# Kernel optimization log

Measured on AMD Instinct MI355X. Metric: run time of the kernel, lower is better.

## Reference

```python
import jax, jax.numpy as jnp
import numpy as np

DIM = 2048      # model dim
H = 32          # num_heads
N = 128         # state_dim
G = 1           # num_groups
K = 4           # conv_size
HID = 4096     # hidden_dim = multiple_of*ceil(2.0*DIM/256)
P = HID // H    # head_dim = 128
CHUNK = 256
EPS = 1e-6
DT_MIN, DT_MAX = 0.001, 0.1


def setup_inputs() -> dict:
    key = jax.random.key(0)
    ks = jax.random.split(key, 8)
    b, s = 2, 2048
    d_in = 2 * HID + 2 * G * N + H           # 8448
    conv_dim = HID + 2 * G * N               # 4352
    return {
        "x": jax.random.normal(ks[0], (b, s, DIM), jnp.float32),
        "W_in": jax.random.normal(ks[1], (d_in, DIM), jnp.float32) / np.sqrt(DIM),
        "conv_w": jax.random.normal(ks[2], (conv_dim, K), jnp.float32) / np.sqrt(K),
        "conv_b": jnp.zeros((conv_dim,), jnp.float32),
        "dt_bias": jnp.zeros((H,), jnp.float32),
        "A_log": jnp.log(jax.random.uniform(ks[3], (H,), jnp.float32, 1.0, 16.0)),
        "D": jnp.ones((H,), jnp.float32),
        "norm_w": jnp.ones((HID,), jnp.float32),
        "W_out": jax.random.normal(ks[4], (DIM, HID), jnp.float32) / np.sqrt(HID),
    }


def _causal_conv_silu(xBC, w, bias):
    # depthwise causal conv1d, kernel K, then SiLU. xBC: (b,s,c), w: (c,K)
    b, s, c = xBC.shape
    xp = jnp.pad(xBC, ((0, 0), (K - 1, 0), (0, 0)))
    y = sum(xp[:, k:k + s, :] * w[:, k] for k in range(K)) + bias
    return jax.nn.silu(y)


def _chunked_scan(x, dt, A, B, C, D):
    # Mamba2 chunked selective scan.
    # x:(b,s,h,p) dt:(b,s,h) A:(h,) B,C:(b,s,n) (groups=1) D:(h,)
    b, s, h, p = x.shape
    n = B.shape[-1]
    nc, L = s // CHUNK, CHUNK
    xc = x.reshape(b, nc, L, h, p)
    dtc = dt.reshape(b, nc, L, h)
    Bc = B.reshape(b, nc, L, n)
    Cc = C.reshape(b, nc, L, n)

    dA = dtc * A                          # (b,nc,L,h), A<0
    dA_cs = jnp.cumsum(dA, axis=2)        # (b,nc,L,h)

    # intra-chunk contribution
    seg = dA_cs[:, :, :, None, :] - dA_cs[:, :, None, :, :]   # (b,nc,L,L,h)
    mask = jnp.tril(jnp.ones((L, L), bool))[None, None, :, :, None]
    decay = jnp.exp(jnp.where(mask, seg, -jnp.inf))
    CB = jnp.einsum('bcln,bcsn->bcls', Cc, Bc)                # (b,nc,L,L)
    y_intra = jnp.einsum('bcls,bclsh,bcsh,bcshp->bclhp', CB, decay, dtc, xc)

    # per-chunk final states
    decay_states = jnp.exp(dA_cs[:, :, -1:, :] - dA_cs)       # (b,nc,L,h)
    states = jnp.einsum('bclh,bclh,bclhp,bcln->bchpn', decay_states, dtc, xc, Bc)

    # inter-chunk recurrence over chunk index
    dA_chunk = dA_cs[:, :, -1, :]                              # (b,nc,h)
    def step(prev, inp):
        st, dec = inp
        new = prev * jnp.exp(dec)[:, :, None, None] + st
        return new, prev
    init = jnp.zeros((b, h, p, n), x.dtype)
    _, prev_states = jax.lax.scan(step, init,
                                  (jnp.moveaxis(states, 1, 0), jnp.moveaxis(dA_chunk, 1, 0)))
    prev_states = jnp.moveaxis(prev_states, 0, 1)              # state at start of each chunk

    y_inter = jnp.einsum('bcln,bclh,bchpn->bclhp', Cc, jnp.exp(dA_cs), prev_states)
    y = (y_intra + y_inter).reshape(b, s, h, p)
    return y + x * D[None, None, :, None]


def reference(x, W_in, conv_w, conv_b, dt_bias, A_log, D, norm_w, W_out):
    b, s, _ = x.shape
    zxbcdt = x @ W_in.T                                        # (b,s,2*HID+2GN+H)
    z, xBC, dt = jnp.split(zxbcdt, [HID, 2 * HID + 2 * G * N], axis=-1)
    xBC = _causal_conv_silu(xBC, conv_w, conv_b)
    xs, B, C = jnp.split(xBC, [HID, HID + G * N], axis=-1)
    A = -jnp.exp(A_log)
    dt = jnp.clip(jax.nn.softplus(dt + dt_bias), DT_MIN, DT_MAX)
    xs = xs.reshape(b, s, H, P)
    y = _chunked_scan(xs, dt, A, B, C, D).reshape(b, s, HID)
    y = y * jax.nn.silu(z)                                     # gate, norm_before_gate=False
    y = y * jax.lax.rsqrt(jnp.mean(y * y, axis=-1, keepdims=True) + EPS) * norm_w
    return y @ W_out.T
```

## Files before the change

kernel.cpp:

```cpp
#include <hip/hip_runtime.h>


typedef short s16x8 __attribute__((ext_vector_type(8)));
typedef float f32x4 __attribute__((ext_vector_type(4)));

__device__ __forceinline__ float bf2f(ushort u) {
    return __builtin_bit_cast(float, (unsigned)u << 16);
}
__device__ __forceinline__ ushort f2bf(float f) {
    unsigned u = __builtin_bit_cast(unsigned, f);
    unsigned r = u + 0x7fffu + ((u >> 16) & 1u);
    return (ushort)(r >> 16);
}

__device__ __forceinline__ void gld16(const void* g, void* l) {
    __builtin_amdgcn_global_load_lds((__attribute__((address_space(1))) void*)g,
                                     (__attribute__((address_space(3))) void*)l, 16, 0, 0);
}

#define BARRIER() asm volatile("s_barrier" ::: "memory")

__global__ void cast_all_k(const float4* __restrict__ x, const float4* __restrict__ wout,
                           const float4* __restrict__ win, ushort* __restrict__ xb,
                           ushort* __restrict__ woutb, ushort* __restrict__ winb) {
    const long b = blockIdx.x, tid = threadIdx.x;
    if (b < 8192) {
        long i = b * 256 + tid;
        float4 v = x[i];
        ushort4 o = { f2bf(v.x), f2bf(v.y), f2bf(v.z), f2bf(v.w) };
        *(ushort4*)(xb + i * 4) = o;
    } else if (b < 16384) {
        long i = (b - 8192) * 256 + tid;
        float4 v = wout[i];
        ushort4 o = { f2bf(v.x), f2bf(v.y), f2bf(v.z), f2bf(v.w) };
        *(ushort4*)(woutb + i * 4) = o;
    } else {
        long i = (b - 16384) * 256 + tid;
        ushort4 o;
        if (i < 4341760L) {
            float4 v = win[i];
            o = { f2bf(v.x), f2bf(v.y), f2bf(v.z), f2bf(v.w) };
        } else {
            o = { 0, 0, 0, 0 };
        }
        *(ushort4*)(winb + i * 4) = o;
    }
}

__global__ __launch_bounds__(512, 1) void gemm1_k(const ushort* __restrict__ A,
                                                  const ushort* __restrict__ Bm,
                                                  ushort* __restrict__ zbuf,
                                                  ushort* __restrict__ xbc,
                                                  ushort* __restrict__ dtr) {
    constexpr int K = 2048, NT = 64;
    __shared__ ushort lds[3 * 8192 + 3 * 6144];
    const int tid = threadIdx.x, lane = tid & 63, wave = tid >> 6;
    const int wm = wave >> 2, wn = wave & 3;
    const int bid = blockIdx.x;
    const int xcd = bid & 7, w = bid >> 3;
    const int mt = xcd * 2 + (w & 1), nt = w >> 1;
    const long m0 = (long)mt * 256, n0 = (long)nt * 192;

    const int st_row = lane >> 2;
    const int st_gc = ((lane & 3) * 8) ^ (((lane >> 5) & 1) << 4);

    auto STAGE_A = [&](int buf, int kt) {
#pragma unroll
        for (int j = 0; j < 2; j++) {
            int sidx = wave + j * 8;
            gld16(A + (m0 + sidx * 16 + st_row) * K + kt + st_gc,
                  lds + buf * 8192 + sidx * 512 + lane * 8);
        }
    };
    auto STAGE_B = [&](int buf, int kt) {
#pragma unroll
        for (int j = 0; j < 2; j++) {
            int sidx = wave + j * 8;
            if (sidx < 12)
                gld16(Bm + (n0 + sidx * 16 + st_row) * K + kt + st_gc,
                      lds + 24576 + buf * 6144 + sidx * 512 + lane * 8);
        }
    };

    const int cfr = (lane >> 4) * 8;
    const int lr = lane & 15;
    auto LDFA = [&](int buf, int r) -> s16x8 {
        int off = buf * 8192 + ((r >> 4) << 9) + ((r & 15) << 5)
                + (cfr ^ (((r >> 3) & 1) << 4));
        return *(const s16x8*)(lds + off);
    };
    auto LDFB = [&](int buf, int r) -> s16x8 {
        int off = 24576 + buf * 6144 + ((r >> 4) << 9) + ((r & 15) << 5)
                + (cfr ^ (((r >> 3) & 1) << 4));
        return *(const s16x8*)(lds + off);
    };

    f32x4 zero = { 0.f, 0.f, 0.f, 0.f };
    f32x4 acc[8][3];
#pragma unroll
    for (int i = 0; i < 8; i++)
#pragma unroll
        for (int j = 0; j < 3; j++) acc[i][j] = zero;

    STAGE_A(0, 0);  STAGE_B(0, 0);
    STAGE_A(1, 32); STAGE_B(1, 32);
    asm volatile("s_waitcnt vmcnt(3)" ::: "memory");
    BARRIER();

    for (int t = 0; t < NT; ++t) {
        const int cur = t % 3;
        const int nxt = (t + 2) % 3;
        const int kt2 = (t + 2) * 32;
        const bool do_stage = (t + 2) < NT;

        s16x8 bfr[3], alo[4], ahi[4];
#pragma unroll
        for (int ni = 0; ni < 3; ni++) bfr[ni] = LDFB(cur, wn * 48 + ni * 16 + lr);
#pragma unroll
        for (int mi = 0; mi < 4; mi++) alo[mi] = LDFA(cur, wm * 128 + mi * 16 + lr);
#pragma unroll
        for (int mi = 0; mi < 4; mi++) ahi[mi] = LDFA(cur, wm * 128 + 64 + mi * 16 + lr);
        if (do_stage) { STAGE_A(nxt, kt2); STAGE_B(nxt, kt2); }

        __builtin_amdgcn_s_setprio(1);
#pragma unroll
        for (int mi = 0; mi < 4; mi++)
#pragma unroll
            for (int ni = 0; ni < 3; ni++)
                acc[mi][ni] = __builtin_amdgcn_mfma_f32_16x16x32_bf16(alo[mi], bfr[ni], acc[mi][ni], 0, 0, 0);
#pragma unroll
        for (int mi = 0; mi < 4; mi++)
#pragma unroll
            for (int ni = 0; ni < 3; ni++)
                acc[mi + 4][ni] = __builtin_amdgcn_mfma_f32_16x16x32_bf16(ahi[mi], bfr[ni], acc[mi + 4][ni], 0, 0, 0);
        __builtin_amdgcn_s_setprio(0);

        if (do_stage) asm volatile("s_waitcnt vmcnt(3)" ::: "memory");
        else          asm volatile("s_waitcnt vmcnt(0)" ::: "memory");
        BARRIER();
    }

    const int lr4 = (lane >> 4) * 4;
#pragma unroll
    for (int mi = 0; mi < 8; mi++) {
#pragma unroll
        for (int ni = 0; ni < 3; ni++) {
            const long col = n0 + wn * 48 + ni * 16 + lr;
            ushort* dst;
            long stride;
            if (col < 4096)      { dst = zbuf + col;         stride = 4096; }
            else if (col < 8448) { dst = xbc + (col - 4096); stride = 4352; }
            else if (col < 8480) { dst = dtr + (col - 8448); stride = 32;   }
            else continue;
            const long row0 = m0 + wm * 128 + mi * 16 + lr4;
#pragma unroll
            for (int r = 0; r < 4; r++) dst[(row0 + r) * stride] = f2bf(acc[mi][ni][r]);
        }
    }
}

__global__ __launch_bounds__(512, 1) void gemm2_k(const ushort* __restrict__ A,
                                                  const ushort* __restrict__ Bm,
                                                  float* __restrict__ Cout) {
    constexpr int K = 4096, NT = 128;
    __shared__ ushort lds[3 * 8192 + 3 * 4096];
    const int tid = threadIdx.x, lane = tid & 63, wave = tid >> 6;
    const int wm = wave >> 2, wn = wave & 3;
    const int bid = blockIdx.x;
    const int xcd = bid & 7, w = bid >> 3;
    const int mt = xcd * 2 + (w & 1), nt = w >> 1;
    const long m0 = (long)mt * 256, n0 = (long)nt * 128;

    const int st_row = lane >> 2;
    const int st_gc = ((lane & 3) * 8) ^ (((lane >> 5) & 1) << 4);

    auto STAGE_A = [&](int buf, int kt) {
#pragma unroll
        for (int j = 0; j < 2; j++) {
            int sidx = wave + j * 8;
            gld16(A + (m0 + sidx * 16 + st_row) * K + kt + st_gc,
                  lds + buf * 8192 + sidx * 512 + lane * 8);
        }
    };
    auto STAGE_B = [&](int buf, int kt) {
        int sidx = wave;
        gld16(Bm + (n0 + sidx * 16 + st_row) * K + kt + st_gc,
              lds + 24576 + buf * 4096 + sidx * 512 + lane * 8);
    };

    const int cfr = (lane >> 4) * 8;
    const int lr = lane & 15;
    auto LDFA = [&](int buf, int r) -> s16x8 {
        int off = buf * 8192 + ((r >> 4) << 9) + ((r & 15) << 5)
                + (cfr ^ (((r >> 3) & 1) << 4));
        return *(const s16x8*)(lds + off);
    };
    auto LDFB = [&](int buf, int r) -> s16x8 {
        int off = 24576 + buf * 4096 + ((r >> 4) << 9) + ((r & 15) << 5)
                + (cfr ^ (((r >> 3) & 1) << 4));
        return *(const s16x8*)(lds + off);
    };

    f32x4 zero = { 0.f, 0.f, 0.f, 0.f };
    f32x4 acc[8][2];
#pragma unroll
    for (int i = 0; i < 8; i++)
#pragma unroll
        for (int j = 0; j < 2; j++) acc[i][j] = zero;

    STAGE_A(0, 0);  STAGE_B(0, 0);
    STAGE_A(1, 32); STAGE_B(1, 32);
    asm volatile("s_waitcnt vmcnt(2)" ::: "memory");
    BARRIER();

    for (int t = 0; t < NT; ++t) {
        const int cur = t % 3;
        const int nxt = (t + 2) % 3;
        const int kt2 = (t + 2) * 32;
        const bool do_stage = (t + 2) < NT;

        s16x8 bfr[2], alo[4], ahi[4];
#pragma unroll
        for (int ni = 0; ni < 2; ni++) bfr[ni] = LDFB(cur, wn * 32 + ni * 16 + lr);
#pragma unroll
        for (int mi = 0; mi < 4; mi++) alo[mi] = LDFA(cur, wm * 128 + mi * 16 + lr);
#pragma unroll
        for (int mi = 0; mi < 4; mi++) ahi[mi] = LDFA(cur, wm * 128 + 64 + mi * 16 + lr);
        if (do_stage) { STAGE_A(nxt, kt2); STAGE_B(nxt, kt2); }

        __builtin_amdgcn_s_setprio(1);
#pragma unroll
        for (int mi = 0; mi < 4; mi++)
#pragma unroll
            for (int ni = 0; ni < 2; ni++)
                acc[mi][ni] = __builtin_amdgcn_mfma_f32_16x16x32_bf16(alo[mi], bfr[ni], acc[mi][ni], 0, 0, 0);
#pragma unroll
        for (int mi = 0; mi < 4; mi++)
#pragma unroll
            for (int ni = 0; ni < 2; ni++)
                acc[mi + 4][ni] = __builtin_amdgcn_mfma_f32_16x16x32_bf16(ahi[mi], bfr[ni], acc[mi + 4][ni], 0, 0, 0);
        __builtin_amdgcn_s_setprio(0);

        if (do_stage) asm volatile("s_waitcnt vmcnt(2)" ::: "memory");
        else          asm volatile("s_waitcnt vmcnt(0)" ::: "memory");
        BARRIER();
    }

    const int lr4 = (lane >> 4) * 4;
#pragma unroll
    for (int mi = 0; mi < 8; mi++) {
#pragma unroll
        for (int ni = 0; ni < 2; ni++) {
            const long col = n0 + wn * 32 + ni * 16 + lr;
            const long row0 = m0 + wm * 128 + mi * 16 + lr4;
#pragma unroll
            for (int r = 0; r < 4; r++)
                Cout[(row0 + r) * 2048 + col] = acc[mi][ni][r];
        }
    }
}

__global__ __launch_bounds__(256) void convx_k(const ushort* __restrict__ xbc,
                                               const float* __restrict__ w,
                                               const float* __restrict__ bias,
                                               ushort* __restrict__ xbcc,
                                               ushort* __restrict__ xT,
                                               ushort* __restrict__ Bt) {
    __shared__ ushort xin[35][136];
    __shared__ ushort yL[32][132];
    const int stile = blockIdx.x, slot = blockIdx.y, bc = blockIdx.z;
    const int tid = threadIdx.x;
    const int cc = bc & 7;
    const long tbase = (long)bc * 256 + stile * 32;
    const int c0 = slot * 128;
    const bool head = (cc == 0 && stile == 0);

#pragma unroll
    for (int i = 0; i < 3; i++) {
        int u = tid + i * 256;
        if (u < 560) {
            int r = u >> 4, seg = u & 15;
            s16x8 v;
            if (head && r < 3) {
#pragma unroll
                for (int j = 0; j < 8; j++) v[j] = 0;
            } else {
                v = *(const s16x8*)&xbc[(tbase - 3 + r) * 4352 + c0 + seg * 8];
            }
            *(s16x8*)&xin[r][seg * 8] = v;
        }
    }
    __syncthreads();

    const int s_loc = tid >> 3, p0 = (tid & 7) * 16;
    ushort yo[16];
#pragma unroll
    for (int j = 0; j < 16; j++) {
        int c = p0 + j;
        float a = bias[c0 + c];
#pragma unroll
        for (int k = 0; k < 4; k++)
            a += bf2f(xin[s_loc + k][c]) * w[(c0 + c) * 4 + k];
        float yv = a / (1.f + __expf(-a));
        ushort ub = f2bf(yv);
        yo[j] = ub;
        yL[s_loc][c] = ub;
    }
    *(s16x8*)&xbcc[(tbase + s_loc) * 4352 + c0 + p0] = *(const s16x8*)&yo[0];
    *(s16x8*)&xbcc[(tbase + s_loc) * 4352 + c0 + p0 + 8] = *(const s16x8*)&yo[8];
    __syncthreads();

    if (slot < 33) {
        const int p = tid >> 1, s0 = (tid & 1) * 16;
        ushort o[16];
#pragma unroll
        for (int j = 0; j < 16; j++) o[j] = yL[s0 + j][p];
        ushort* dst = (slot < 32)
            ? (xT + ((long)(bc * 32 + slot) * 128 + p) * 256 + stile * 32 + s0)
            : (Bt + ((long)bc * 128 + p) * 256 + stile * 32 + s0);
        *(s16x8*)&dst[0] = *(const s16x8*)&o[0];
        *(s16x8*)&dst[8] = *(const s16x8*)&o[8];
    }
}

__global__ void prep_k(const ushort* __restrict__ dtr, const float* __restrict__ dt_bias,
                       const float* __restrict__ A_log, float* __restrict__ dtp,
                       float* __restrict__ dacs) {
    const int bx = blockIdx.x;
    const int h = bx & 31, cc = (bx >> 5) & 7, bi = bx >> 8;
    const int lane = threadIdx.x;
    const float A = -__expf(A_log[h]);
    const float bsh = dt_bias[h];
    float v[4], cs[4];
    float run = 0.f;
#pragma unroll
    for (int j = 0; j < 4; j++) {
        int pos = cc * 256 + lane * 4 + j;
        float raw = bf2f(dtr[((long)(bi * 2048 + pos)) * 32 + h]) + bsh;
        float sp = (raw > 20.f) ? raw : log1pf(__expf(raw));
        float d = fminf(fmaxf(sp, 0.001f), 0.1f);
        v[j] = d;
        run += d * A;
        cs[j] = run;
    }
    float tot = run, pre = run;
    for (int off = 1; off < 64; off <<= 1) {
        float u = __shfl_up(pre, off, 64);
        if (lane >= off) pre += u;
    }
    float excl = pre - tot;
    const long base = ((long)(bi * 32 + h)) * 2048 + cc * 256 + lane * 4;
#pragma unroll
    for (int j = 0; j < 4; j++) { dtp[base + j] = v[j]; dacs[base + j] = excl + cs[j]; }
}

__global__ __launch_bounds__(256) void cb_mfma_k(const ushort* __restrict__ xbcc,
                                                 float* __restrict__ CB) {
    const int bid = blockIdx.x;
    const int sq = bid & 1, lq = (bid >> 1) & 1, bc = bid >> 2;
    const int tid = threadIdx.x, lane = tid & 63, wave = tid >> 6;
    const int wm = wave >> 1, wn = wave & 1;
    const long tbase = (long)bc * 256;

    f32x4 zero = { 0.f, 0.f, 0.f, 0.f };
    f32x4 acc[4][4];
#pragma unroll
    for (int i = 0; i < 4; i++)
#pragma unroll
        for (int j = 0; j < 4; j++) acc[i][j] = zero;

    for (int kst = 0; kst < 4; ++kst) {
        const int koff = kst * 32 + (lane >> 4) * 8;
        s16x8 a[4], b[4];
#pragma unroll
        for (int mi = 0; mi < 4; mi++) {
            int l = lq * 128 + wm * 64 + mi * 16 + (lane & 15);
            a[mi] = *(const s16x8*)&xbcc[(tbase + l) * 4352 + 4224 + koff];
        }
#pragma unroll
        for (int ni = 0; ni < 4; ni++) {
            int s = sq * 128 + wn * 64 + ni * 16 + (lane & 15);
            b[ni] = *(const s16x8*)&xbcc[(tbase + s) * 4352 + 4096 + koff];
        }
#pragma unroll
        for (int mi = 0; mi < 4; mi++)
#pragma unroll
            for (int ni = 0; ni < 4; ni++)
                acc[mi][ni] = __builtin_amdgcn_mfma_f32_16x16x32_bf16(a[mi], b[ni], acc[mi][ni], 0, 0, 0);
    }

    float* out = CB + (long)bc * 65536;
#pragma unroll
    for (int mi = 0; mi < 4; mi++)
#pragma unroll
        for (int ni = 0; ni < 4; ni++)
#pragma unroll
            for (int r = 0; r < 4; r++) {
                int l = lq * 128 + wm * 64 + mi * 16 + (lane >> 4) * 4 + r;
                int s = sq * 128 + wn * 64 + ni * 16 + (lane & 15);
                out[(long)l * 256 + s] = acc[mi][ni][r];
            }
}

__global__ __launch_bounds__(256) void scan_mfma_k(const ushort* __restrict__ xT,
                                                   const float* __restrict__ CB,
                                                   const float* __restrict__ dtp,
                                                   const float* __restrict__ dacs,
                                                   const ushort* __restrict__ xbcc,
                                                   const float* __restrict__ st,
                                                   float* __restrict__ yf) {
    const int bx = blockIdx.x;
    const int ltile = bx & 1, h = (bx >> 1) & 31, cc = (bx >> 6) & 7, bi = bx >> 9;
    const int tid = threadIdx.x, lane = tid & 63, wave = tid >> 6;
    const int wm = wave >> 1, wn = wave & 1;

    __shared__ float dA_s[256];
    __shared__ float F_s[256];

    const long dbase = ((long)(bi * 32 + h)) * 2048 + cc * 256;
    {
        float a = dacs[dbase + tid];
        float r = dacs[dbase + (tid | 31)];
        dA_s[tid] = a;
        F_s[tid] = __expf(r - a) * dtp[dbase + tid];
    }
    __syncthreads();

    int lch[4];
    float dAl[4];
#pragma unroll
    for (int mi = 0; mi < 4; mi++) {
        lch[mi] = ltile * 128 + wm * 64 + mi * 16 + (lane & 15);
        dAl[mi] = dA_s[lch[mi]];
    }

    f32x4 zero = { 0.f, 0.f, 0.f, 0.f };
    f32x4 acc[4][4];
#pragma unroll
    for (int i = 0; i < 4; i++)
#pragma unroll
        for (int j = 0; j < 4; j++) acc[i][j] = zero;

    const long tbase = (long)bi * 2048 + cc * 256;
    const long cbbase = ((long)(bi * 8 + cc)) * 65536;
    const ushort* xrow = xT + (((long)(bi * 8 + cc) * 32 + h) * 128) * 256;
    const int nsb = ltile * 4 + 4;

    for (int sb = 0; sb < nsb; ++sb) {
        const int soff = sb * 32 + (lane >> 4) * 8;
        s16x8 bf[4];
#pragma unroll
        for (int ni = 0; ni < 4; ni++) {
            int p = wn * 64 + ni * 16 + (lane & 15);
            bf[ni] = *(const s16x8*)&xrow[(long)p * 256 + soff];
        }
        const float Rsb = dA_s[sb * 32 + 31];
        const int s0 = soff;
#pragma unroll
        for (int mi = 0; mi < 4; mi++) {
            const int lb = lch[mi] >> 5;
            if (sb > lb) continue;
            const float* cbrow = CB + cbbase + (long)lch[mi] * 256 + s0;
            float4 c0 = *(const float4*)cbrow;
            float4 c1 = *(const float4*)(cbrow + 4);
            float E = __expf(dAl[mi] - Rsb);
            float m[8];
            m[0] = c0.x * E * F_s[s0 + 0]; m[1] = c0.y * E * F_s[s0 + 1];
            m[2] = c0.z * E * F_s[s0 + 2]; m[3] = c0.w * E * F_s[s0 + 3];
            m[4] = c1.x * E * F_s[s0 + 4]; m[5] = c1.y * E * F_s[s0 + 5];
            m[6] = c1.z * E * F_s[s0 + 6]; m[7] = c1.w * E * F_s[s0 + 7];
            if (sb == lb) {
#pragma unroll
                for (int j = 0; j < 8; j++)
                    if (s0 + j > lch[mi]) m[j] = 0.f;
            }
            s16x8 a;
#pragma unroll
            for (int j = 0; j < 8; j++) a[j] = (short)f2bf(m[j]);
#pragma unroll
            for (int ni = 0; ni < 4; ni++)
                acc[mi][ni] = __builtin_amdgcn_mfma_f32_16x16x32_bf16(a, bf[ni], acc[mi][ni], 0, 0, 0);
        }
    }

    const float* sbase = st + (((long)(bi * 8 + cc) * 32 + h) * 128) * 128;
    float eAr[4];
#pragma unroll
    for (int mi = 0; mi < 4; mi++) eAr[mi] = __expf(dAl[mi]);
    for (int kk = 0; kk < 4; ++kk) {
        const int koff = kk * 32 + (lane >> 4) * 8;
        s16x8 a[4], b[4];
#pragma unroll
        for (int mi = 0; mi < 4; mi++) {
            s16x8 raw = *(const s16x8*)&xbcc[(tbase + lch[mi]) * 4352 + 4224 + koff];
#pragma unroll
            for (int j = 0; j < 8; j++)
                a[mi][j] = (short)f2bf(bf2f((ushort)raw[j]) * eAr[mi]);
        }
#pragma unroll
        for (int ni = 0; ni < 4; ni++) {
            int p = wn * 64 + ni * 16 + (lane & 15);
            const float* pr = sbase + (long)p * 128 + koff;
            float4 v0 = *(const float4*)pr;
            float4 v1 = *(const float4*)(pr + 4);
            b[ni][0] = (short)f2bf(v0.x); b[ni][1] = (short)f2bf(v0.y);
            b[ni][2] = (short)f2bf(v0.z); b[ni][3] = (short)f2bf(v0.w);
            b[ni][4] = (short)f2bf(v1.x); b[ni][5] = (short)f2bf(v1.y);
            b[ni][6] = (short)f2bf(v1.z); b[ni][7] = (short)f2bf(v1.w);
        }
#pragma unroll
        for (int mi = 0; mi < 4; mi++)
#pragma unroll
            for (int ni = 0; ni < 4; ni++)
                acc[mi][ni] = __builtin_amdgcn_mfma_f32_16x16x32_bf16(a[mi], b[ni], acc[mi][ni], 0, 0, 0);
    }

    const long crow = tbase + ltile * 128 + wm * 64 + ((lane >> 4) << 2);
    const int ccol = h * 128 + wn * 64 + (lane & 15);
#pragma unroll
    for (int mi = 0; mi < 4; mi++)
#pragma unroll
        for (int ni = 0; ni < 4; ni++)
#pragma unroll
            for (int r = 0; r < 4; r++)
                yf[(crow + mi * 16 + r) * 4096 + ccol + ni * 16] = acc[mi][ni][r];
}

__global__ __launch_bounds__(256) void states_mfma_k(const ushort* __restrict__ xT,
                                                     const ushort* __restrict__ Bt,
                                                     const float* __restrict__ dtp,
                                                     const float* __restrict__ dacs,
                                                     float* __restrict__ states) {
    const int bx = blockIdx.x;
    const int h = bx & 31, cc = (bx >> 5) & 7, bi = bx >> 8;
    const int bc = bi * 8 + cc;
    const int tid = threadIdx.x, lane = tid & 63, wave = tid >> 6;
    const int wm = wave >> 1, wn = wave & 1;
    __shared__ float wl[256];
    const long dbase = ((long)(bi * 32 + h)) * 2048 + cc * 256;
    {
        float last = dacs[dbase + 255];
        wl[tid] = __expf(last - dacs[dbase + tid]) * dtp[dbase + tid];
    }
    __syncthreads();

    f32x4 zero = { 0.f, 0.f, 0.f, 0.f };
    f32x4 acc[4][4];
#pragma unroll
    for (int i = 0; i < 4; i++)
#pragma unroll
        for (int j = 0; j < 4; j++) acc[i][j] = zero;

    const ushort* xrow = xT + (((long)bc * 32 + h) * 128) * 256;
    const ushort* brow = Bt + ((long)bc * 128) * 256;

    for (int sb = 0; sb < 8; ++sb) {
        const int soff = sb * 32 + (lane >> 4) * 8;
        s16x8 a[4], b[4];
#pragma unroll
        for (int mi = 0; mi < 4; mi++) {
            int p = wm * 64 + mi * 16 + (lane & 15);
            s16x8 raw = *(const s16x8*)&xrow[(long)p * 256 + soff];
#pragma unroll
            for (int j = 0; j < 8; j++)
                a[mi][j] = (short)f2bf(bf2f((ushort)raw[j]) * wl[soff + j]);
        }
#pragma unroll
        for (int ni = 0; ni < 4; ni++) {
            int n = wn * 64 + ni * 16 + (lane & 15);
            b[ni] = *(const s16x8*)&brow[(long)n * 256 + soff];
        }
#pragma unroll
        for (int mi = 0; mi < 4; mi++)
#pragma unroll
            for (int ni = 0; ni < 4; ni++)
                acc[mi][ni] = __builtin_amdgcn_mfma_f32_16x16x32_bf16(a[mi], b[ni], acc[mi][ni], 0, 0, 0);
    }

    float* out = states + (((long)bc * 32 + h) * 128) * 128;
#pragma unroll
    for (int mi = 0; mi < 4; mi++)
#pragma unroll
        for (int ni = 0; ni < 4; ni++)
#pragma unroll
            for (int r = 0; r < 4; r++) {
                int p = wm * 64 + mi * 16 + (lane >> 4) * 4 + r;
                int n = wn * 64 + ni * 16 + (lane & 15);
                out[(long)p * 128 + n] = acc[mi][ni][r];
            }
}

__global__ void rec_k(float* __restrict__ states, const float* __restrict__ dacs) {
    const int i = blockIdx.x * 256 + threadIdx.x;
    const int n = i & 127, p = (i >> 7) & 127, h = (i >> 14) & 31, bi = i >> 19;
    const long dbase = ((long)(bi * 32 + h)) * 2048;
    float run = 0.f;
    for (int cc = 0; cc < 8; cc++) {
        const long off = ((((long)(bi * 8 + cc)) * 32 + h) * 128 + p) * 128 + n;
        float st = states[off];
        states[off] = run;
        float dec = dacs[dbase + cc * 256 + 255];
        run = run * __expf(dec) + st;
    }
}

__global__ __launch_bounds__(256) void gate_rms_k(const float* __restrict__ y, const ushort* __restrict__ zbuf,
                                                  const ushort* __restrict__ xbcc, const float* __restrict__ Dv,
                                                  const float* __restrict__ norm_w, ushort* __restrict__ yb) {
    const int t = blockIdx.x, tid = threadIdx.x;
    const float* yr = &y[(long)t * 4096];
    const ushort* zr = &zbuf[(long)t * 4096];
    const ushort* xr = &xbcc[(long)t * 4352];
    float g[16];
    float ss = 0.f;
#pragma unroll
    for (int j = 0; j < 16; j++) {
        int i = j * 256 + tid;
        float z = bf2f(zr[i]);
        float yv = yr[i] + Dv[i >> 7] * bf2f(xr[i]);
        float gv = yv * (z / (1.f + __expf(-z)));
        g[j] = gv;
        ss += gv * gv;
    }
#pragma unroll
    for (int off = 32; off > 0; off >>= 1) ss += __shfl_xor(ss, off, 64);
    __shared__ float red[4];
    if ((tid & 63) == 0) red[tid >> 6] = ss;
    __syncthreads();
    float tot = red[0] + red[1] + red[2] + red[3];
    float sc = rsqrtf(tot * (1.f / 4096.f) + 1e-6f);
#pragma unroll
    for (int j = 0; j < 16; j++) {
        int i = j * 256 + tid;
        yb[(long)t * 4096 + i] = f2bf(g[j] * sc * norm_w[i]);
    }
}

extern "C" void kernel_launch(void* const* d_in, const int* in_sizes, int n_in,
                              void* d_out, int out_size, void* d_ws, size_t ws_size,
                              hipStream_t stream) {
    const float* x       = (const float*)d_in[0];
    const float* W_in    = (const float*)d_in[1];
    const float* conv_w  = (const float*)d_in[2];
    const float* conv_b  = (const float*)d_in[3];
    const float* dt_bias = (const float*)d_in[4];
    const float* A_log   = (const float*)d_in[5];
    const float* Dv      = (const float*)d_in[6];
    const float* norm_w  = (const float*)d_in[7];
    const float* W_out   = (const float*)d_in[8];

    char* w8 = (char*)d_ws;
    ushort* xb    = (ushort*)(w8 + 0L);
    ushort* xT    = (ushort*)(w8 + 0L);
    ushort* yb    = (ushort*)(w8 + 0L);
    ushort* woutb = (ushort*)(w8 + 33554432L);
    ushort* Bt    = (ushort*)(w8 + 50331648L);
    ushort* zbuf  = (ushort*)(w8 + 52428800L);
    ushort* xbc   = (ushort*)(w8 + 85983232L);
    ushort* dtr   = (ushort*)(w8 + 121634816L);
    ushort* xbcc  = (ushort*)(w8 + 121896960L);
    float*  dtp   = (float*)(w8 + 157548544L);
    float*  dacs  = (float*)(w8 + 158072832L);
    float*  cb    = (float*)(w8 + 158597120L);
    float*  yf    = (float*)(w8 + 162791424L);
    ushort* winb  = (ushort*)(w8 + 162791424L);
    float*  st    = (float*)(w8 + 229900288L);

    cast_all_k<<<34048, 256, 0, stream>>>((const float4*)x, (const float4*)W_out,
                                          (const float4*)W_in, xb, woutb, winb);
    gemm1_k<<<736, 512, 0, stream>>>(xb, winb, zbuf, xbc, dtr);
    convx_k<<<dim3(8, 34, 16), 256, 0, stream>>>(xbc, conv_w, conv_b, xbcc, xT, Bt);
    prep_k<<<512, 64, 0, stream>>>(dtr, dt_bias, A_log, dtp, dacs);
    cb_mfma_k<<<64, 256, 0, stream>>>(xbcc, cb);
    states_mfma_k<<<512, 256, 0, stream>>>(xT, Bt, dtp, dacs, st);
    rec_k<<<4096, 256, 0, stream>>>(st, dacs);
    scan_mfma_k<<<1024, 256, 0, stream>>>(xT, cb, dtp, dacs, xbcc, st, yf);
    gate_rms_k<<<4096, 256, 0, stream>>>(yf, zbuf, xbcc, Dv, norm_w, yb);
    gemm2_k<<<256, 512, 0, stream>>>(yb, woutb, (float*)d_out);
}
```

Before: 465.1 us.

## Deepen GEMM LDS pipeline to four stages and double-buffer register fragments

Both projection GEMMs move from a 3-stage to a 4-stage LDS ring buffer, prefetching three K-tiles ahead. They also read the next tile's fragments from LDS into a second register set while MFMAs run on the current set. This is meant to hide global-load and LDS-read latency behind matrix math. The cost is more LDS and more VGPRs for the second fragment set, which may raise register pressure. Wait counts are now tuned per wave because of the uneven B-tile load split.

```diff
diff --git a/kernel.cpp b/kernel.cpp
--- a/kernel.cpp
+++ b/kernel.cpp
@@ -53,7 +53,7 @@
                                                   ushort* __restrict__ xbc,
                                                   ushort* __restrict__ dtr) {
     constexpr int K = 2048, NT = 64;
-    __shared__ ushort lds[3 * 8192 + 3 * 6144];
+    __shared__ ushort lds[4 * 8192 + 4 * 6144];
     const int tid = threadIdx.x, lane = tid & 63, wave = tid >> 6;
     const int wm = wave >> 2, wn = wave & 3;
     const int bid = blockIdx.x;
@@ -64,21 +64,19 @@
     const int st_row = lane >> 2;
     const int st_gc = ((lane & 3) * 8) ^ (((lane >> 5) & 1) << 4);
 
-    auto STAGE_A = [&](int buf, int kt) {
+    auto STAGE = [&](int buf, int kt) {
 #pragma unroll
         for (int j = 0; j < 2; j++) {
             int sidx = wave + j * 8;
             gld16(A + (m0 + sidx * 16 + st_row) * K + kt + st_gc,
                   lds + buf * 8192 + sidx * 512 + lane * 8);
         }
-    };
-    auto STAGE_B = [&](int buf, int kt) {
 #pragma unroll
         for (int j = 0; j < 2; j++) {
             int sidx = wave + j * 8;
             if (sidx < 12)
                 gld16(Bm + (n0 + sidx * 16 + st_row) * K + kt + st_gc,
-                      lds + 24576 + buf * 6144 + sidx * 512 + lane * 8);
+                      lds + 32768 + buf * 6144 + sidx * 512 + lane * 8);
         }
     };
 
@@ -90,10 +88,18 @@
         return *(const s16x8*)(lds + off);
     };
     auto LDFB = [&](int buf, int r) -> s16x8 {
-        int off = 24576 + buf * 6144 + ((r >> 4) << 9) + ((r & 15) << 5)
+        int off = 32768 + buf * 6144 + ((r >> 4) << 9) + ((r & 15) << 5)
                 + (cfr ^ (((r >> 3) & 1) << 4));
         return *(const s16x8*)(lds + off);
     };
+    auto RDFRAGS = [&](int buf, s16x8 (&f)[11]) {
+#pragma unroll
+        for (int ni = 0; ni < 3; ni++) f[ni] = LDFB(buf, wn * 48 + ni * 16 + lr);
+#pragma unroll
+        for (int mi = 0; mi < 4; mi++) f[3 + mi] = LDFA(buf, wm * 128 + mi * 16 + lr);
+#pragma unroll
+        for (int mi = 0; mi < 4; mi++) f[7 + mi] = LDFA(buf, wm * 128 + 64 + mi * 16 + lr);
+    };
 
     f32x4 zero = { 0.f, 0.f, 0.f, 0.f };
     f32x4 acc[8][3];
@@ -102,42 +108,45 @@
 #pragma unroll
         for (int j = 0; j < 3; j++) acc[i][j] = zero;
 
-    STAGE_A(0, 0);  STAGE_B(0, 0);
-    STAGE_A(1, 32); STAGE_B(1, 32);
-    asm volatile("s_waitcnt vmcnt(3)" ::: "memory");
+    auto MFMAS = [&](s16x8 (&f)[11]) {
+        __builtin_amdgcn_s_setprio(1);
+#pragma unroll
+        for (int mi = 0; mi < 4; mi++)
+#pragma unroll
+            for (int ni = 0; ni < 3; ni++)
+                acc[mi][ni] = __builtin_amdgcn_mfma_f32_16x16x32_bf16(f[3 + mi], f[ni], acc[mi][ni], 0, 0, 0);
+#pragma unroll
+        for (int mi = 0; mi < 4; mi++)
+#pragma unroll
+            for (int ni = 0; ni < 3; ni++)
+                acc[mi + 4][ni] = __builtin_amdgcn_mfma_f32_16x16x32_bf16(f[7 + mi], f[ni], acc[mi + 4][ni], 0, 0, 0);
+        __builtin_amdgcn_s_setprio(0);
+    };
+    auto VWAIT = [&](bool tail) {
+        if (tail)           { asm volatile("s_waitcnt vmcnt(0)" ::: "memory"); }
+        else if (wave < 4)  { asm volatile("s_waitcnt vmcnt(4)" ::: "memory"); }
+        else                { asm volatile("s_waitcnt vmcnt(3)" ::: "memory"); }
+    };
+
+    s16x8 fc[11], fn[11];
+
+    STAGE(0, 0); STAGE(1, 32); STAGE(2, 64);
+    VWAIT(false);
     BARRIER();
-
-    for (int t = 0; t < NT; ++t) {
-        const int cur = t % 3;
-        const int nxt = (t + 2) % 3;
-        const int kt2 = (t + 2) * 32;
-        const bool do_stage = (t + 2) < NT;
-
-        s16x8 bfr[3], alo[4], ahi[4];
-#pragma unroll
-        for (int ni = 0; ni < 3; ni++) bfr[ni] = LDFB(cur, wn * 48 + ni * 16 + lr);
-#pragma unroll
-        for (int mi = 0; mi < 4; mi++) alo[mi] = LDFA(cur, wm * 128 + mi * 16 + lr);
-#pragma unroll
-        for (int mi = 0; mi < 4; mi++) ahi[mi] = LDFA(cur, wm * 128 + 64 + mi * 16 + lr);
-        if (do_stage) { STAGE_A(nxt, kt2); STAGE_B(nxt, kt2); }
-
-        __builtin_amdgcn_s_setprio(1);
-#pragma unroll
-        for (int mi = 0; mi < 4; mi++)
-#pragma unroll
-            for (int ni = 0; ni < 3; ni++)
-                acc[mi][ni] = __builtin_amdgcn_mfma_f32_16x16x32_bf16(alo[mi], bfr[ni], acc[mi][ni], 0, 0, 0);
-#pragma unroll
-        for (int mi = 0; mi < 4; mi++)
-#pragma unroll
-            for (int ni = 0; ni < 3; ni++)
-                acc[mi + 4][ni] = __builtin_amdgcn_mfma_f32_16x16x32_bf16(ahi[mi], bfr[ni], acc[mi + 4][ni], 0, 0, 0);
-        __builtin_amdgcn_s_setprio(0);
-
-        if (do_stage) asm volatile("s_waitcnt vmcnt(3)" ::: "memory");
-        else          asm volatile("s_waitcnt vmcnt(0)" ::: "memory");
+    RDFRAGS(0, fc);
+
+    auto TILE = [&](int t, s16x8 (&cur)[11], s16x8 (&nxt)[11]) {
+        const bool do_stage = (t + 3) < NT;
+        if (do_stage) STAGE((t + 3) & 3, (t + 3) * 32);
+        if ((t + 1) < NT) RDFRAGS((t + 1) & 3, nxt);
+        MFMAS(cur);
+        VWAIT(!do_stage);
         BARRIER();
+    };
+
+    for (int t = 0; t < NT; t += 2) {
+        TILE(t, fc, fn);
+        TILE(t + 1, fn, fc);
     }
 
     const int lr4 = (lane >> 4) * 4;
@@ -163,7 +172,7 @@
                                                   const ushort* __restrict__ Bm,
                                                   float* __restrict__ Cout) {
     constexpr int K = 4096, NT = 128;
-    __shared__ ushort lds[3 * 8192 + 3 * 4096];
+    __shared__ ushort lds[4 * 8192 + 4 * 4096];
     const int tid = threadIdx.x, lane = tid & 63, wave = tid >> 6;
     const int wm = wave >> 2, wn = wave & 3;
     const int bid = blockIdx.x;
@@ -174,18 +183,15 @@
     const int st_row = lane >> 2;
     const int st_gc = ((lane & 3) * 8) ^ (((lane >> 5) & 1) << 4);
 
-    auto STAGE_A = [&](int buf, int kt) {
+    auto STAGE = [&](int buf, int kt) {
 #pragma unroll
         for (int j = 0; j < 2; j++) {
             int sidx = wave + j * 8;
             gld16(A + (m0 + sidx * 16 + st_row) * K + kt + st_gc,
                   lds + buf * 8192 + sidx * 512 + lane * 8);
         }
-    };
-    auto STAGE_B = [&](int buf, int kt) {
-        int sidx = wave;
-        gld16(Bm + (n0 + sidx * 16 + st_row) * K + kt + st_gc,
-              lds + 24576 + buf * 4096 + sidx * 512 + lane * 8);
+        gld16(Bm + (n0 + wave * 16 + st_row) * K + kt + st_gc,
+              lds + 32768 + buf * 4096 + wave * 512 + lane * 8);
     };
 
     const int cfr = (lane >> 4) * 8;
@@ -196,10 +202,18 @@
         return *(const s16x8*)(lds + off);
     };
     auto LDFB = [&](int buf, int r) -> s16x8 {
-        int off = 24576 + buf * 4096 + ((r >> 4) << 9) + ((r & 15) << 5)
+        int off = 32768 + buf * 4096 + ((r >> 4) << 9) + ((r & 15) << 5)
                 + (cfr ^ (((r >> 3) & 1) << 4));
         return *(const s16x8*)(lds + off);
     };
+    auto RDFRAGS = [&](int buf, s16x8 (&f)[10]) {
+#pragma unroll
+        for (int ni = 0; ni < 2; ni++) f[ni] = LDFB(buf, wn * 32 + ni * 16 + lr);
+#pragma unroll
+        for (int mi = 0; mi < 4; mi++) f[2 + mi] = LDFA(buf, wm * 128 + mi * 16 + lr);
+#pragma unroll
+        for (int mi = 0; mi < 4; mi++) f[6 + mi] = LDFA(buf, wm * 128 + 64 + mi * 16 + lr);
+    };
 
     f32x4 zero = { 0.f, 0.f, 0.f, 0.f };
     f32x4 acc[8][2];
@@ -208,42 +222,44 @@
 #pragma unroll
         for (int j = 0; j < 2; j++) acc[i][j] = zero;
 
-    STAGE_A(0, 0);  STAGE_B(0, 0);
-    STAGE_A(1, 32); STAGE_B(1, 32);
-    asm volatile("s_waitcnt vmcnt(2)" ::: "memory");
+    auto MFMAS = [&](s16x8 (&f)[10]) {
+        __builtin_amdgcn_s_setprio(1);
+#pragma unroll
+        for (int mi = 0; mi < 4; mi++)
+#pragma unroll
+            for (int ni = 0; ni < 2; ni++)
+                acc[mi][ni] = __builtin_amdgcn_mfma_f32_16x16x32_bf16(f[2 + mi], f[ni], acc[mi][ni], 0, 0, 0);
+#pragma unroll
+        for (int mi = 0; mi < 4; mi++)
+#pragma unroll
+            for (int ni = 0; ni < 2; ni++)
+                acc[mi + 4][ni] = __builtin_amdgcn_mfma_f32_16x16x32_bf16(f[6 + mi], f[ni], acc[mi + 4][ni], 0, 0, 0);
+        __builtin_amdgcn_s_setprio(0);
+    };
+    auto VWAIT = [&](bool tail) {
+        if (tail) { asm volatile("s_waitcnt vmcnt(0)" ::: "memory"); }
+        else      { asm volatile("s_waitcnt vmcnt(3)" ::: "memory"); }
+    };
+
+    s16x8 fc[10], fn[10];
+
+    STAGE(0, 0); STAGE(1, 32); STAGE(2, 64);
+    VWAIT(false);
     BARRIER();
-
-    for (int t = 0; t < NT; ++t) {
-        const int cur = t % 3;
-        const int nxt = (t + 2) % 3;
-        const int kt2 = (t + 2) * 32;
-        const bool do_stage = (t + 2) < NT;
-
-        s16x8 bfr[2], alo[4], ahi[4];
-#pragma unroll
-        for (int ni = 0; ni < 2; ni++) bfr[ni] = LDFB(cur, wn * 32 + ni * 16 + lr);
-#pragma unroll
-        for (int mi = 0; mi < 4; mi++) alo[mi] = LDFA(cur, wm * 128 + mi * 16 + lr);
-#pragma unroll
-        for (int mi = 0; mi < 4; mi++) ahi[mi] = LDFA(cur, wm * 128 + 64 + mi * 16 + lr);
-        if (do_stage) { STAGE_A(nxt, kt2); STAGE_B(nxt, kt2); }
-
-        __builtin_amdgcn_s_setprio(1);
-#pragma unroll
-        for (int mi = 0; mi < 4; mi++)
-#pragma unroll
-            for (int ni = 0; ni < 2; ni++)
-                acc[mi][ni] = __builtin_amdgcn_mfma_f32_16x16x32_bf16(alo[mi], bfr[ni], acc[mi][ni], 0, 0, 0);
-#pragma unroll
-        for (int mi = 0; mi < 4; mi++)
-#pragma unroll
-            for (int ni = 0; ni < 2; ni++)
-                acc[mi + 4][ni] = __builtin_amdgcn_mfma_f32_16x16x32_bf16(ahi[mi], bfr[ni], acc[mi + 4][ni], 0, 0, 0);
-        __builtin_amdgcn_s_setprio(0);
-
-        if (do_stage) asm volatile("s_waitcnt vmcnt(2)" ::: "memory");
-        else          asm volatile("s_waitcnt vmcnt(0)" ::: "memory");
+    RDFRAGS(0, fc);
+
+    auto TILE = [&](int t, s16x8 (&cur)[10], s16x8 (&nxt)[10]) {
+        const bool do_stage = (t + 3) < NT;
+        if (do_stage) STAGE((t + 3) & 3, (t + 3) * 32);
+        if ((t + 1) < NT) RDFRAGS((t + 1) & 3, nxt);
+        MFMAS(cur);
+        VWAIT(!do_stage);
         BARRIER();
+    };
+
+    for (int t = 0; t < NT; t += 2) {
+        TILE(t, fc, fn);
+        TILE(t + 1, fn, fc);
     }
 
     const int lr4 = (lane >> 4) * 4;
```

Result: no change. 460.3 us (-1.0%).

## Switch GEMMs to double-buffered LDS with higher occupancy and smaller gemm2 tiles

Applied to the files above, without the earlier changes.

Both GEMM kernels drop from triple to double LDS buffering. Staging of the next tile is issued before the fragment loads, and each iteration ends with a full vmcnt(0) wait. Launch bounds are raised so several blocks can share a CU. gemm2 is retiled from 256x128 tiles with 512 threads to 128x128 tiles with 256 threads, doubling its grid to 512 blocks. The goal is to hide latency through occupancy rather than deep in-block prefetch, at the cost of less prefetch distance, possible register pressure under the tighter bounds, and less data reuse per block in gemm2.

```diff
diff --git a/kernel.cpp b/kernel.cpp
--- a/kernel.cpp
+++ b/kernel.cpp
@@ -47,13 +47,13 @@
     }
 }
 
-__global__ __launch_bounds__(512, 1) void gemm1_k(const ushort* __restrict__ A,
+__global__ __launch_bounds__(512, 4) void gemm1_k(const ushort* __restrict__ A,
                                                   const ushort* __restrict__ Bm,
                                                   ushort* __restrict__ zbuf,
                                                   ushort* __restrict__ xbc,
                                                   ushort* __restrict__ dtr) {
     constexpr int K = 2048, NT = 64;
-    __shared__ ushort lds[3 * 8192 + 3 * 6144];
+    __shared__ ushort lds[2 * 8192 + 2 * 6144];
     const int tid = threadIdx.x, lane = tid & 63, wave = tid >> 6;
     const int wm = wave >> 2, wn = wave & 3;
     const int bid = blockIdx.x;
@@ -64,21 +64,19 @@
     const int st_row = lane >> 2;
     const int st_gc = ((lane & 3) * 8) ^ (((lane >> 5) & 1) << 4);
 
-    auto STAGE_A = [&](int buf, int kt) {
+    auto STAGE = [&](int buf, int kt) {
 #pragma unroll
         for (int j = 0; j < 2; j++) {
             int sidx = wave + j * 8;
             gld16(A + (m0 + sidx * 16 + st_row) * K + kt + st_gc,
                   lds + buf * 8192 + sidx * 512 + lane * 8);
         }
-    };
-    auto STAGE_B = [&](int buf, int kt) {
 #pragma unroll
         for (int j = 0; j < 2; j++) {
             int sidx = wave + j * 8;
             if (sidx < 12)
                 gld16(Bm + (n0 + sidx * 16 + st_row) * K + kt + st_gc,
-                      lds + 24576 + buf * 6144 + sidx * 512 + lane * 8);
+                      lds + 16384 + buf * 6144 + sidx * 512 + lane * 8);
         }
     };
 
@@ -90,7 +88,7 @@
         return *(const s16x8*)(lds + off);
     };
     auto LDFB = [&](int buf, int r) -> s16x8 {
-        int off = 24576 + buf * 6144 + ((r >> 4) << 9) + ((r & 15) << 5)
+        int off = 16384 + buf * 6144 + ((r >> 4) << 9) + ((r & 15) << 5)
                 + (cfr ^ (((r >> 3) & 1) << 4));
         return *(const s16x8*)(lds + off);
     };
@@ -102,16 +100,13 @@
 #pragma unroll
         for (int j = 0; j < 3; j++) acc[i][j] = zero;
 
-    STAGE_A(0, 0);  STAGE_B(0, 0);
-    STAGE_A(1, 32); STAGE_B(1, 32);
-    asm volatile("s_waitcnt vmcnt(3)" ::: "memory");
+    STAGE(0, 0);
+    asm volatile("s_waitcnt vmcnt(0)" ::: "memory");
     BARRIER();
 
     for (int t = 0; t < NT; ++t) {
-        const int cur = t % 3;
-        const int nxt = (t + 2) % 3;
-        const int kt2 = (t + 2) * 32;
-        const bool do_stage = (t + 2) < NT;
+        const int cur = t & 1;
+        if ((t + 1) < NT) STAGE((t + 1) & 1, (t + 1) * 32);
 
         s16x8 bfr[3], alo[4], ahi[4];
 #pragma unroll
@@ -120,7 +115,6 @@
         for (int mi = 0; mi < 4; mi++) alo[mi] = LDFA(cur, wm * 128 + mi * 16 + lr);
 #pragma unroll
         for (int mi = 0; mi < 4; mi++) ahi[mi] = LDFA(cur, wm * 128 + 64 + mi * 16 + lr);
-        if (do_stage) { STAGE_A(nxt, kt2); STAGE_B(nxt, kt2); }
 
         __builtin_amdgcn_s_setprio(1);
 #pragma unroll
@@ -135,8 +129,7 @@
                 acc[mi + 4][ni] = __builtin_amdgcn_mfma_f32_16x16x32_bf16(ahi[mi], bfr[ni], acc[mi + 4][ni], 0, 0, 0);
         __builtin_amdgcn_s_setprio(0);
 
-        if (do_stage) asm volatile("s_waitcnt vmcnt(3)" ::: "memory");
-        else          asm volatile("s_waitcnt vmcnt(0)" ::: "memory");
+        asm volatile("s_waitcnt vmcnt(0)" ::: "memory");
         BARRIER();
     }
 
@@ -159,105 +152,91 @@
     }
 }
 
-__global__ __launch_bounds__(512, 1) void gemm2_k(const ushort* __restrict__ A,
+__global__ __launch_bounds__(256, 4) void gemm2_k(const ushort* __restrict__ A,
                                                   const ushort* __restrict__ Bm,
                                                   float* __restrict__ Cout) {
     constexpr int K = 4096, NT = 128;
-    __shared__ ushort lds[3 * 8192 + 3 * 4096];
+    __shared__ ushort lds[2 * 4096 + 2 * 4096];
     const int tid = threadIdx.x, lane = tid & 63, wave = tid >> 6;
-    const int wm = wave >> 2, wn = wave & 3;
+    const int wm = wave >> 1, wn = wave & 1;
     const int bid = blockIdx.x;
     const int xcd = bid & 7, w = bid >> 3;
-    const int mt = xcd * 2 + (w & 1), nt = w >> 1;
-    const long m0 = (long)mt * 256, n0 = (long)nt * 128;
+    const int mt = xcd * 4 + (w & 3), nt = w >> 2;
+    const long m0 = (long)mt * 128, n0 = (long)nt * 128;
 
     const int st_row = lane >> 2;
     const int st_gc = ((lane & 3) * 8) ^ (((lane >> 5) & 1) << 4);
 
-    auto STAGE_A = [&](int buf, int kt) {
+    auto STAGE = [&](int buf, int kt) {
 #pragma unroll
         for (int j = 0; j < 2; j++) {
-            int sidx = wave + j * 8;
+            int sidx = wave + j * 4;
             gld16(A + (m0 + sidx * 16 + st_row) * K + kt + st_gc,
-                  lds + buf * 8192 + sidx * 512 + lane * 8);
-        }
-    };
-    auto STAGE_B = [&](int buf, int kt) {
-        int sidx = wave;
-        gld16(Bm + (n0 + sidx * 16 + st_row) * K + kt + st_gc,
-              lds + 24576 + buf * 4096 + sidx * 512 + lane * 8);
+                  lds + buf * 4096 + sidx * 512 + lane * 8);
+        }
+#pragma unroll
+        for (int j = 0; j < 2; j++) {
+            int sidx = wave + j * 4;
+            gld16(Bm + (n0 + sidx * 16 + st_row) * K + kt + st_gc,
+                  lds + 8192 + buf * 4096 + sidx * 512 + lane * 8);
+        }
     };
 
     const int cfr = (lane >> 4) * 8;
     const int lr = lane & 15;
     auto LDFA = [&](int buf, int r) -> s16x8 {
-        int off = buf * 8192 + ((r >> 4) << 9) + ((r & 15) << 5)
+        int off = buf * 4096 + ((r >> 4) << 9) + ((r & 15) << 5)
                 + (cfr ^ (((r >> 3) & 1) << 4));
         return *(const s16x8*)(lds + off);
     };
     auto LDFB = [&](int buf, int r) -> s16x8 {
-        int off = 24576 + buf * 4096 + ((r >> 4) << 9) + ((r & 15) << 5)
+        int off = 8192 + buf * 4096 + ((r >> 4) << 9) + ((r & 15) << 5)
                 + (cfr ^ (((r >> 3) & 1) << 4));
         return *(const s16x8*)(lds + off);
     };
 
     f32x4 zero = { 0.f, 0.f, 0.f, 0.f };
-    f32x4 acc[8][2];
-#pragma unroll
-    for (int i = 0; i < 8; i++)
-#pragma unroll
-        for (int j = 0; j < 2; j++) acc[i][j] = zero;
-
-    STAGE_A(0, 0);  STAGE_B(0, 0);
-    STAGE_A(1, 32); STAGE_B(1, 32);
-    asm volatile("s_waitcnt vmcnt(2)" ::: "memory");
+    f32x4 acc[4][4];
+#pragma unroll
+    for (int i = 0; i < 4; i++)
+#pragma unroll
+        for (int j = 0; j < 4; j++) acc[i][j] = zero;
+
+    STAGE(0, 0);
+    asm volatile("s_waitcnt vmcnt(0)" ::: "memory");
     BARRIER();
 
     for (int t = 0; t < NT; ++t) {
-        const int cur = t % 3;
-        const int nxt = (t + 2) % 3;
-        const int kt2 = (t + 2) * 32;
-        const bool do_stage = (t + 2) < NT;
-
-        s16x8 bfr[2], alo[4], ahi[4];
-#pragma unroll
-        for (int ni = 0; ni < 2; ni++) bfr[ni] = LDFB(cur, wn * 32 + ni * 16 + lr);
-#pragma unroll
-        for (int mi = 0; mi < 4; mi++) alo[mi] = LDFA(cur, wm * 128 + mi * 16 + lr);
-#pragma unroll
-        for (int mi = 0; mi < 4; mi++) ahi[mi] = LDFA(cur, wm * 128 + 64 + mi * 16 + lr);
-        if (do_stage) { STAGE_A(nxt, kt2); STAGE_B(nxt, kt2); }
+        const int cur = t & 1;
+        if ((t + 1) < NT) STAGE((t + 1) & 1, (t + 1) * 32);
+
+        s16x8 af[4], bf[4];
+#pragma unroll
+        for (int mi = 0; mi < 4; mi++) af[mi] = LDFA(cur, wm * 64 + mi * 16 + lr);
+#pragma unroll
+        for (int ni = 0; ni < 4; ni++) bf[ni] = LDFB(cur, wn * 64 + ni * 16 + lr);
 
         __builtin_amdgcn_s_setprio(1);
 #pragma unroll
         for (int mi = 0; mi < 4; mi++)
 #pragma unroll
-            for (int ni = 0; ni < 2; ni++)
-                acc[mi][ni] = __builtin_amdgcn_mfma_f32_16x16x32_bf16(alo[mi], bfr[ni], acc[mi][ni], 0, 0, 0);
-#pragma unroll
-        for (int mi = 0; mi < 4; mi++)
-#pragma unroll
-            for (int ni = 0; ni < 2; ni++)
-                acc[mi + 4][ni] = __builtin_amdgcn_mfma_f32_16x16x32_bf16(ahi[mi], bfr[ni], acc[mi + 4][ni], 0, 0, 0);
+            for (int ni = 0; ni < 4; ni++)
+                acc[mi][ni] = __builtin_amdgcn_mfma_f32_16x16x32_bf16(af[mi], bf[ni], acc[mi][ni], 0, 0, 0);
         __builtin_amdgcn_s_setprio(0);
 
-        if (do_stage) asm volatile("s_waitcnt vmcnt(2)" ::: "memory");
-        else          asm volatile("s_waitcnt vmcnt(0)" ::: "memory");
+        asm volatile("s_waitcnt vmcnt(0)" ::: "memory");
         BARRIER();
     }
 
-    const int lr4 = (lane >> 4) * 4;
-#pragma unroll
-    for (int mi = 0; mi < 8; mi++) {
-#pragma unroll
-        for (int ni = 0; ni < 2; ni++) {
-            const long col = n0 + wn * 32 + ni * 16 + lr;
-            const long row0 = m0 + wm * 128 + mi * 16 + lr4;
+    const long crow = m0 + wm * 64 + ((lane >> 4) << 2);
+    const long ccol = n0 + wn * 64 + (lane & 15);
+#pragma unroll
+    for (int mi = 0; mi < 4; mi++)
+#pragma unroll
+        for (int ni = 0; ni < 4; ni++)
 #pragma unroll
             for (int r = 0; r < 4; r++)
-                Cout[(row0 + r) * 2048 + col] = acc[mi][ni][r];
-        }
-    }
+                Cout[(crow + mi * 16 + r) * 2048 + ccol + ni * 16] = acc[mi][ni][r];
 }
 
 __global__ __launch_bounds__(256) void convx_k(const ushort* __restrict__ xbc,
@@ -676,5 +655,5 @@
     rec_k<<<4096, 256, 0, stream>>>(st, dacs);
     scan_mfma_k<<<1024, 256, 0, stream>>>(xT, cb, dtp, dacs, xbcc, st, yf);
     gate_rms_k<<<4096, 256, 0, stream>>>(yf, zbuf, xbcc, Dv, norm_w, yb);
-    gemm2_k<<<256, 512, 0, stream>>>(yb, woutb, (float*)d_out);
-}
+    gemm2_k<<<512, 256, 0, stream>>>(yb, woutb, (float*)d_out);
+}
```

Result: slower. 1.081 ms (+132.4%).
